# Performance work log

Measured on AMD Instinct MI355X. Metric: run time of the kernel, lower is better.

## Reference

```python
import jax, jax.numpy as jnp
import numpy as np

B, S, D, H = 1, 2048, 1024, 16
HD = D // H  # head_dim = 64
ROPE_BASE = 10000.0


def _rope_cos_sin(seqlen, head_dim, dtype):
    inv_freq = 1.0 / (ROPE_BASE ** (jnp.arange(0, head_dim, 2, dtype=jnp.float32) / head_dim))
    t = jnp.arange(seqlen, dtype=jnp.float32)
    freqs = jnp.outer(t, inv_freq)                      # [S, HD/2]
    emb = jnp.concatenate([freqs, freqs], axis=-1)      # [S, HD]
    # broadcast shape [1, S, 1, HD] over (batch, seq, heads, head_dim)
    return jnp.cos(emb)[None, :, None, :].astype(dtype), jnp.sin(emb)[None, :, None, :].astype(dtype)


def _rotate_half(x):
    x1, x2 = jnp.split(x, 2, axis=-1)
    return jnp.concatenate([-x2, x1], axis=-1)


def setup_inputs() -> dict:
    key = jax.random.key(0)
    k1, k2, k3 = jax.random.split(key, 3)
    std_in = 1.0 / np.sqrt(D)
    std_out = std_in / np.sqrt(2.0)  # layer_id = 0
    x = jax.random.normal(k1, (B, S, D), dtype=jnp.float32)
    w_in = jax.random.normal(k2, (3 * H * HD, D), dtype=jnp.float32) * std_in
    w_out = jax.random.normal(k3, (D, H * HD), dtype=jnp.float32) * std_out
    return {"x": x, "w_in": w_in, "w_out": w_out, "is_causal": 1}


def reference(x, w_in, w_out, is_causal):
    b, s, _ = x.shape
    qkv = jnp.einsum('bsd,ed->bse', x, w_in)            # [B,S,3*H*HD]
    xq, xk, xv = jnp.split(qkv, 3, axis=-1)
    xq = xq.reshape(b, s, H, HD)
    xk = xk.reshape(b, s, H, HD)
    xv = xv.reshape(b, s, H, HD)
    cos, sin = _rope_cos_sin(s, HD, xq.dtype)
    xq = xq * cos + _rotate_half(xq) * sin
    xk = xk * cos + _rotate_half(xk) * sin
    scale = 1.0 / np.sqrt(HD)
    scores = jnp.einsum('bqhd,bkhd->bhqk', xq, xk) * scale  # [B,H,S,S]
    if is_causal:
        mask = jnp.tril(jnp.ones((s, s), dtype=bool))
        scores = jnp.where(mask[None, None], scores, jnp.finfo(scores.dtype).min)
    probs = jax.nn.softmax(scores, axis=-1)
    out = jnp.einsum('bhqk,bkhd->bqhd', probs, xv)      # [B,S,H,HD]
    out = out.reshape(b, s, H * HD)
    return jnp.einsum('bse,de->bsd', out, w_out)
```

## Files before the change

kernel.cpp:

```cpp
#include <hip/hip_runtime.h>
#include <stdint.h>

#define S_LEN 2048
#define DMODEL 1024
#define NHEAD 16
#define HDIM 64
#define NE 3072
#define C2 0.18033688011112042f
#define RINV (-13.287712379549449f / 32.f)

typedef __attribute__((ext_vector_type(8))) short short8_t;
typedef __attribute__((ext_vector_type(4))) float f32x4;
typedef __attribute__((ext_vector_type(16))) float f32x16;

__device__ __forceinline__ float bf2f(ushort u) {
  union { float f; uint32_t i; } c; c.i = ((uint32_t)u) << 16; return c.f;
}
__device__ __forceinline__ ushort f2bf(float f) {
  union { float f; uint32_t i; } c; c.f = f;
  uint32_t x = c.i;
  return (ushort)((x + 0x7fffu + ((x >> 16) & 1u)) >> 16);
}

__device__ __forceinline__ void gload_lds16(const ushort* g, ushort* l) {
  __builtin_amdgcn_global_load_lds(
      (const __attribute__((address_space(1))) void*)g,
      (__attribute__((address_space(3))) void*)l, 16, 0, 0);
}

__global__ void cvt_all(const float* __restrict__ x, const float* __restrict__ w_in,
                        const float* __restrict__ w_out,
                        ushort* __restrict__ xbf, ushort* __restrict__ winbf,
                        ushort* __restrict__ woutbf) {
  int i = blockIdx.x * blockDim.x + threadIdx.x;
  const float* src; ushort* dst; int off;
  if (i < 524288)       { src = x;     dst = xbf;    off = i; }
  else if (i < 1310720) { src = w_in;  dst = winbf;  off = i - 524288; }
  else                  { src = w_out; dst = woutbf; off = i - 1310720; }
  float4 v = ((const float4*)src)[off];
  ushort4 o;
  o.x = f2bf(v.x); o.y = f2bf(v.y); o.z = f2bf(v.z); o.w = f2bf(v.w);
  ((ushort4*)dst)[off] = o;
}

template<int BM, int BN, int MODE>
__global__ __launch_bounds__(256) void gemm_abt(
    const ushort* __restrict__ A, const ushort* __restrict__ B,
    void* __restrict__ Cv, ushort* __restrict__ kfrag, ushort* __restrict__ vfrag,
    int M, int N, int K)
{
  constexpr int AR = BM / 32;
  constexpr int AC = BN / 32;
  constexpr int PG = (BM + BN) / 32;
  __shared__ ushort lds[(BM + BN) * 64];

  const int nbn = N / BN;
  const int cpx = gridDim.x >> 3;
  const int bid = blockIdx.x;
  const int swz = (bid & 7) * cpx + (bid >> 3);
  const int bm = swz / nbn;
  const int bn = swz - bm * nbn;
  const int tid = threadIdx.x;
  const int w = tid >> 6, l = tid & 63;
  const int wm = w >> 1, wn = w & 1;
  const int fr = l & 15, fg = l >> 4;

  f32x4 acc[AR][AC];
#pragma unroll
  for (int r = 0; r < AR; ++r)
#pragma unroll
    for (int c = 0; c < AC; ++c) acc[r][c] = (f32x4){0.f, 0.f, 0.f, 0.f};

  const ushort* gsrc[PG];
  ushort* ldst[PG];
#pragma unroll
  for (int i = 0; i < PG; ++i) {
    int ch = w + 4 * i;
    int row = ch * 8 + (l >> 3);
    if (row < BM)
      gsrc[i] = A + (size_t)(bm * BM + row) * K + (l & 7) * 8;
    else
      gsrc[i] = B + (size_t)(bn * BN + (row - BM)) * K + (l & 7) * 8;
    ldst[i] = &lds[ch * 512];
  }

  const ushort* fa = &lds[(wm * (BM / 2) + fr) * 64 + fg * 8];
  const ushort* fb = &lds[BM * 64 + (wn * (BN / 2) + fr) * 64 + fg * 8];

  for (int k0 = 0; k0 < K; k0 += 64) {
    __syncthreads();
#pragma unroll
    for (int i = 0; i < PG; ++i) gload_lds16(gsrc[i] + k0, ldst[i]);
    __syncthreads();

    short8_t af[AR][2], bfr[AC][2];
#pragma unroll
    for (int r = 0; r < AR; ++r)
#pragma unroll
      for (int kk = 0; kk < 2; ++kk) {
        union { short8_t v; uint4 q; } u;
        u.q = *(const uint4*)(fa + r * 1024 + kk * 32);
        af[r][kk] = u.v;
      }
#pragma unroll
    for (int c = 0; c < AC; ++c)
#pragma unroll
      for (int kk = 0; kk < 2; ++kk) {
        union { short8_t v; uint4 q; } u;
        u.q = *(const uint4*)(fb + c * 1024 + kk * 32);
        bfr[c][kk] = u.v;
      }
    __builtin_amdgcn_s_setprio(1);
#pragma unroll
    for (int kk = 0; kk < 2; ++kk)
#pragma unroll
      for (int r = 0; r < AR; ++r)
#pragma unroll
        for (int c = 0; c < AC; ++c)
          acc[r][c] = __builtin_amdgcn_mfma_f32_16x16x32_bf16(af[r][kk], bfr[c][kk], acc[r][c], 0, 0, 0);
    __builtin_amdgcn_s_setprio(0);
  }

  if constexpr (MODE == 0) {
    const int row0 = bm * BM + wm * (BM / 2) + fg * 4;
    const int col0 = bn * BN + wn * (BN / 2) + fr;
#pragma unroll
    for (int r = 0; r < AR; ++r)
#pragma unroll
      for (int c = 0; c < AC; ++c)
#pragma unroll
        for (int j = 0; j < 4; ++j)
          ((float*)Cv)[(size_t)(row0 + r * 16 + j) * N + col0 + c * 16] = acc[r][c][j];
  } else {
    const int cls = bn >> 4;
    const int h = bn & 15;
    if (cls == 0) {
      const int row0 = bm * BM + wm * (BM / 2) + fg * 4;
      const int colq = bn * 64 + wn * 32 + fr;
      ushort* qb = (ushort*)Cv;
#pragma unroll
      for (int r = 0; r < AR; ++r)
#pragma unroll
        for (int c = 0; c < AC; ++c)
#pragma unroll
          for (int j = 0; j < 4; ++j)
            qb[(size_t)(row0 + r * 16 + j) * 1024 + colq + c * 16] = f2bf(acc[r][c][j]);
    } else {
      __syncthreads();
      ushort* T = lds;
#pragma unroll
      for (int r = 0; r < AR; ++r)
#pragma unroll
        for (int c = 0; c < AC; ++c)
#pragma unroll
          for (int j = 0; j < 4; ++j) {
            int rl = wm * 64 + r * 16 + fg * 4 + j;
            int cl = wn * 32 + c * 16 + fr;
            T[rl * 72 + cl] = f2bf(acc[r][c][j]);
          }
      __syncthreads();

      if (cls == 1) {
        const int ii = tid & 31;
        const float invf = exp2f((float)ii * RINV);
#pragma unroll
        for (int kk = 0; kk < 16; ++kk) {
          int key = (tid >> 5) * 16 + kk;
          float sn, cs;
          sincosf((float)(bm * 128 + key) * invf, &sn, &cs);
          float x1 = bf2f(T[key * 72 + ii]), x2 = bf2f(T[key * 72 + ii + 32]);
          T[key * 72 + ii]      = f2bf(x1 * cs - x2 * sn);
          T[key * 72 + ii + 32] = f2bf(x2 * cs + x1 * sn);
        }
        __syncthreads();
#pragma unroll
        for (int it = 0; it < 4; ++it) {
          int idx = tid + 256 * it;
          int tt = idx >> 9, e = idx & 511;
          int c2 = e >> 6, l2 = e & 63, q2 = l2 & 31, hi2 = l2 >> 5;
          int kh = c2 >> 2, ks = c2 & 3;
          uint4 v = *(const uint4*)&T[(64 * tt + 32 * kh + q2) * 72 + 16 * ks + 8 * hi2];
          *(uint4*)(kfrag + (size_t)(h * 32 + bm * 2 + tt) * 4096 + e * 8) = v;
        }
      } else {
#pragma unroll
        for (int it = 0; it < 4; ++it) {
          int idx = tid + 256 * it;
          int tt = idx >> 9, e = idx & 511;
          int c2 = e >> 6, l2 = e & 63, q2 = l2 & 31, hi2 = l2 >> 5;
          int ks = c2 >> 1, dh = c2 & 1;
          ushort tmp[8];
#pragma unroll
          for (int jj = 0; jj < 8; ++jj)
            tmp[jj] = T[(64 * tt + 16 * ks + 8 * hi2 + jj) * 72 + 32 * dh + q2];
          *(uint4*)(vfrag + (size_t)(h * 32 + bm * 2 + tt) * 4096 + e * 8) = *(const uint4*)tmp;
        }
      }
    }
  }
}

__global__ __launch_bounds__(256) void attn_mfma(
    const ushort* __restrict__ qbuf, const ushort* __restrict__ kfrag,
    const ushort* __restrict__ vfrag, ushort* __restrict__ O,
    const int* __restrict__ icausal)
{
  __shared__ ushort obf[4][32][68];
  __shared__ float2 mdl[4][32];

  const int bid = blockIdx.x;
  const int h = (bid & 7) * 2 + ((bid >> 3) & 1);
  const int i = bid >> 4;
  const int g = i & 15, k = i >> 4;
  const int qt = (k == 0) ? g : (k == 1) ? (63 - g) : (k == 2) ? (31 - g) : (32 + g);

  const int causal = *icausal;
  const int nt = causal ? ((qt >> 1) + 1) : (S_LEN / 64);

  const int tid = threadIdx.x;
  const int w = tid >> 6, l = tid & 63;
  const int q = l & 31, hi = l >> 5;
  const int q0 = qt * 32;
  const int qa = q0 + q;
  const int t0 = w * nt / 4, t1 = (w + 1) * nt / 4;

  short8_t qf[4];
  {
    const ushort* qp = qbuf + (size_t)qa * 1024 + h * HDIM + 8 * hi;
#pragma unroll
    for (int ks = 0; ks < 4; ++ks) {
      union { short8_t v; uint4 u; } uu;
      uu.u = *(const uint4*)(qp + 16 * ks);
      qf[ks] = uu.v;
    }
    union { short8_t v; ushort u[8]; } a0, a1, b0, b1;
    a0.v = qf[0]; a1.v = qf[1]; b0.v = qf[2]; b1.v = qf[3];
#pragma unroll
    for (int j = 0; j < 8; ++j) {
      {
        float invf = exp2f((float)(8 * hi + j) * RINV);
        float sn, cs; sincosf((float)qa * invf, &sn, &cs);
        float x1 = bf2f(a0.u[j]), x2 = bf2f(b0.u[j]);
        a0.u[j] = f2bf(x1 * cs - x2 * sn);
        b0.u[j] = f2bf(x2 * cs + x1 * sn);
      }
      {
        float invf = exp2f((float)(16 + 8 * hi + j) * RINV);
        float sn, cs; sincosf((float)qa * invf, &sn, &cs);
        float x1 = bf2f(a1.u[j]), x2 = bf2f(b1.u[j]);
        a1.u[j] = f2bf(x1 * cs - x2 * sn);
        b1.u[j] = f2bf(x2 * cs + x1 * sn);
      }
    }
    qf[0] = a0.v; qf[1] = a1.v; qf[2] = b0.v; qf[3] = b1.v;
  }

  const ushort* kb = kfrag + (size_t)(h * 32 + t0) * 4096 + l * 8;
  const ushort* vb = vfrag + (size_t)(h * 32 + t0) * 4096 + l * 8;

  float m_run = -1e30f, den = 0.f;
  f32x16 oacc[2];
#pragma unroll
  for (int d = 0; d < 2; ++d)
#pragma unroll
    for (int r = 0; r < 16; ++r) oacc[d][r] = 0.f;

  if (t0 < t1) {
    uint4 kq[8];
#pragma unroll
    for (int ks = 0; ks < 4; ++ks)
#pragma unroll
      for (int kh = 0; kh < 2; ++kh)
        kq[ks * 2 + kh] = *(const uint4*)(kb + (kh * 4 + ks) * 512);
    kb += 4096;

    for (int t = t0; t < t1; ++t) {
      uint4 vq[8];
#pragma unroll
      for (int c = 0; c < 8; ++c)
        vq[c] = *(const uint4*)(vb + c * 512);
      vb += 4096;

      f32x16 sacc[2];
#pragma unroll
      for (int kh = 0; kh < 2; ++kh)
#pragma unroll
        for (int r = 0; r < 16; ++r) sacc[kh][r] = 0.f;
      __builtin_amdgcn_s_setprio(1);
#pragma unroll
      for (int ks = 0; ks < 4; ++ks)
#pragma unroll
        for (int kh = 0; kh < 2; ++kh) {
          union { short8_t v; uint4 u; } ku;
          ku.u = kq[ks * 2 + kh];
          sacc[kh] = __builtin_amdgcn_mfma_f32_32x32x16_bf16(ku.v, qf[ks], sacc[kh], 0, 0, 0);
        }
      __builtin_amdgcn_s_setprio(0);

      if (t + 1 < t1) {
#pragma unroll
        for (int ks = 0; ks < 4; ++ks)
#pragma unroll
          for (int kh = 0; kh < 2; ++kh)
            kq[ks * 2 + kh] = *(const uint4*)(kb + (kh * 4 + ks) * 512);
        kb += 4096;
      }

      if (causal && t == nt - 1) {
        const int k0 = t * 64;
#pragma unroll
        for (int kh = 0; kh < 2; ++kh)
#pragma unroll
          for (int r = 0; r < 16; ++r)
            if (k0 + 32 * kh + (r & 3) + 8 * (r >> 2) + 4 * hi > qa) sacc[kh][r] = -3e38f;
      }

      float v0 = -3e38f, v1 = -3e38f, v2 = -3e38f, v3 = -3e38f;
#pragma unroll
      for (int kh = 0; kh < 2; ++kh)
#pragma unroll
        for (int r = 0; r < 16; r += 4) {
          v0 = fmaxf(v0, sacc[kh][r + 0]);
          v1 = fmaxf(v1, sacc[kh][r + 1]);
          v2 = fmaxf(v2, sacc[kh][r + 2]);
          v3 = fmaxf(v3, sacc[kh][r + 3]);
        }
      float vmax = fmaxf(fmaxf(v0, v1), fmaxf(v2, v3));
      vmax = fmaxf(vmax, __shfl_xor(vmax, 32));

      if (__any(vmax > m_run + 44.3614196f)) {
        float mn = fmaxf(m_run, vmax);
        float alpha = exp2f((m_run - mn) * C2);
        den *= alpha;
#pragma unroll
        for (int d = 0; d < 2; ++d)
#pragma unroll
          for (int r = 0; r < 16; ++r) oacc[d][r] *= alpha;
        m_run = mn;
      }
      float mc2 = m_run * C2;
      float p0 = 0.f, p1 = 0.f, p2 = 0.f, p3 = 0.f;
#pragma unroll
      for (int kh = 0; kh < 2; ++kh)
#pragma unroll
        for (int r = 0; r < 16; r += 4) {
          float e0 = exp2f(fmaf(sacc[kh][r + 0], C2, -mc2));
          float e1 = exp2f(fmaf(sacc[kh][r + 1], C2, -mc2));
          float e2 = exp2f(fmaf(sacc[kh][r + 2], C2, -mc2));
          float e3 = exp2f(fmaf(sacc[kh][r + 3], C2, -mc2));
          sacc[kh][r + 0] = e0; sacc[kh][r + 1] = e1;
          sacc[kh][r + 2] = e2; sacc[kh][r + 3] = e3;
          p0 += e0; p1 += e1; p2 += e2; p3 += e3;
        }
      float psum = (p0 + p1) + (p2 + p3);
      psum += __shfl_xor(psum, 32);
      den += psum;

      short8_t pa[4];
#pragma unroll
      for (int ks = 0; ks < 4; ++ks) {
        const int blk = ks >> 1, kp = (ks & 1) * 8;
        uint wL0, wL1, wH0, wH1;
        asm("v_cvt_pk_bf16_f32 %0, %1, %2" : "=v"(wL0) : "v"(sacc[blk][kp + 0]), "v"(sacc[blk][kp + 1]));
        asm("v_cvt_pk_bf16_f32 %0, %1, %2" : "=v"(wL1) : "v"(sacc[blk][kp + 2]), "v"(sacc[blk][kp + 3]));
        asm("v_cvt_pk_bf16_f32 %0, %1, %2" : "=v"(wH0) : "v"(sacc[blk][kp + 4]), "v"(sacc[blk][kp + 5]));
        asm("v_cvt_pk_bf16_f32 %0, %1, %2" : "=v"(wH1) : "v"(sacc[blk][kp + 6]), "v"(sacc[blk][kp + 7]));
        uint s0 = hi ? wL0 : wH0, s1 = hi ? wL1 : wH1;
        uint r0 = __shfl_xor(s0, 32), r1 = __shfl_xor(s1, 32);
        union { short8_t v; uint u[4]; } pu;
        pu.u[0] = hi ? r0 : wL0;
        pu.u[1] = hi ? r1 : wL1;
        pu.u[2] = hi ? wH0 : r0;
        pu.u[3] = hi ? wH1 : r1;
        pa[ks] = pu.v;
      }

      __builtin_amdgcn_s_setprio(1);
#pragma unroll
      for (int ks = 0; ks < 4; ++ks)
#pragma unroll
        for (int dh = 0; dh < 2; ++dh) {
          union { short8_t v; uint4 u; } vu;
          vu.u = vq[ks * 2 + dh];
          oacc[dh] = __builtin_amdgcn_mfma_f32_32x32x16_bf16(vu.v, pa[ks], oacc[dh], 0, 0, 0);
        }
      __builtin_amdgcn_s_setprio(0);
    }
  }

#pragma unroll
  for (int dh = 0; dh < 2; ++dh)
#pragma unroll
    for (int rq = 0; rq < 4; ++rq) {
      uint a0, a1;
      asm("v_cvt_pk_bf16_f32 %0, %1, %2" : "=v"(a0) : "v"(oacc[dh][4 * rq + 0]), "v"(oacc[dh][4 * rq + 1]));
      asm("v_cvt_pk_bf16_f32 %0, %1, %2" : "=v"(a1) : "v"(oacc[dh][4 * rq + 2]), "v"(oacc[dh][4 * rq + 3]));
      uint2 dd; dd.x = a0; dd.y = a1;
      *(uint2*)&obf[w][q][32 * dh + 8 * rq + 4 * hi] = dd;
    }
  if (hi == 0) mdl[w][q] = make_float2(m_run, den);
  __syncthreads();

  {
    const int qq = tid >> 3, d8 = tid & 7;
    float2 md0 = mdl[0][qq], md1 = mdl[1][qq], md2 = mdl[2][qq], md3 = mdl[3][qq];
    float mt = fmaxf(fmaxf(md0.x, md1.x), fmaxf(md2.x, md3.x));
    float w0 = exp2f((md0.x - mt) * C2);
    float w1 = exp2f((md1.x - mt) * C2);
    float w2 = exp2f((md2.x - mt) * C2);
    float w3 = exp2f((md3.x - mt) * C2);
    float inv = 1.f / (md0.y * w0 + md1.y * w1 + md2.y * w2 + md3.y * w3);

    uint4 a = *(const uint4*)&obf[0][qq][d8 * 8];
    uint4 b = *(const uint4*)&obf[1][qq][d8 * 8];
    uint4 c = *(const uint4*)&obf[2][qq][d8 * 8];
    uint4 d = *(const uint4*)&obf[3][qq][d8 * 8];
    const ushort* ap = (const ushort*)&a;
    const ushort* bp = (const ushort*)&b;
    const ushort* cp = (const ushort*)&c;
    const ushort* dp = (const ushort*)&d;
    ushort out8[8];
#pragma unroll
    for (int e = 0; e < 8; ++e) {
      float acc = bf2f(ap[e]) * w0 + bf2f(bp[e]) * w1 + bf2f(cp[e]) * w2 + bf2f(dp[e]) * w3;
      out8[e] = f2bf(acc * inv);
    }
    *(uint4*)(O + (size_t)(q0 + qq) * DMODEL + h * HDIM + d8 * 8) = *(const uint4*)out8;
  }
}

extern "C" void kernel_launch(void* const* d_in, const int* in_sizes, int n_in,
                              void* d_out, int out_size, void* d_ws, size_t ws_size,
                              hipStream_t stream) {
  const float* x     = (const float*)d_in[0];
  const float* w_in  = (const float*)d_in[1];
  const float* w_out = (const float*)d_in[2];
  const int* icausal = (const int*)d_in[3];

  char* ws = (char*)d_ws;
  ushort* xbf    = (ushort*)(ws);
  ushort* winbf  = (ushort*)(ws + 4194304);
  ushort* woutbf = (ushort*)(ws + 10485760);
  ushort* qbuf   = (ushort*)(ws + 12582912);
  ushort* kfrag  = (ushort*)(ws + 16777216);
  ushort* vfrag  = (ushort*)(ws + 20971520);
  ushort* obuf   = (ushort*)(ws + 25165824);

  cvt_all<<<6144, 256, 0, stream>>>(x, w_in, w_out, xbf, winbf, woutbf);

  gemm_abt<128, 64, 2><<<16 * 48, 256, 0, stream>>>(xbf, winbf, (void*)qbuf, kfrag, vfrag, 2048, 3072, 1024);
  attn_mfma<<<1024, 256, 0, stream>>>(qbuf, kfrag, vfrag, obuf, icausal);
  gemm_abt<64, 64, 0><<<32 * 16, 256, 0, stream>>>(obuf, woutbf, d_out, nullptr, nullptr, 2048, 1024, 1024);
}
```

Before: 81.49 us.

## Software-pipeline QK^T MFMA for next tile with softmax and PV of current

Restructures the attention inner loop so the QK^T MFMAs for tile t+1 are issued after the softmax of tile t and before its PV MFMAs. The K fragments for tile t+2 and the V fragments for tile t+1 are prefetched further ahead. The exp2 computation is folded into the bf16 packing loop to shorten live ranges. Launch bounds now request two blocks per CU. The aim is to overlap matrix-core work with the exp/shuffle softmax ALU work and to hide global load latency, at the cost of more live registers (sacc, kq and vq all held across the iteration).

```diff
diff --git a/kernel.cpp b/kernel.cpp
--- a/kernel.cpp
+++ b/kernel.cpp
@@ -200,7 +200,7 @@
   }
 }
 
-__global__ __launch_bounds__(256) void attn_mfma(
+__global__ __launch_bounds__(256, 2) void attn_mfma(
     const ushort* __restrict__ qbuf, const ushort* __restrict__ kfrag,
     const ushort* __restrict__ vfrag, ushort* __restrict__ O,
     const int* __restrict__ icausal)
@@ -266,45 +266,45 @@
     for (int r = 0; r < 16; ++r) oacc[d][r] = 0.f;
 
   if (t0 < t1) {
-    uint4 kq[8];
+    uint4 kq[8], vq[8];
 #pragma unroll
     for (int ks = 0; ks < 4; ++ks)
 #pragma unroll
       for (int kh = 0; kh < 2; ++kh)
         kq[ks * 2 + kh] = *(const uint4*)(kb + (kh * 4 + ks) * 512);
     kb += 4096;
+#pragma unroll
+    for (int c = 0; c < 8; ++c)
+      vq[c] = *(const uint4*)(vb + c * 512);
+    vb += 4096;
+
+    f32x16 sacc[2];
+#pragma unroll
+    for (int kh = 0; kh < 2; ++kh)
+#pragma unroll
+      for (int r = 0; r < 16; ++r) sacc[kh][r] = 0.f;
+    __builtin_amdgcn_s_setprio(1);
+#pragma unroll
+    for (int ks = 0; ks < 4; ++ks)
+#pragma unroll
+      for (int kh = 0; kh < 2; ++kh) {
+        union { short8_t v; uint4 u; } ku;
+        ku.u = kq[ks * 2 + kh];
+        sacc[kh] = __builtin_amdgcn_mfma_f32_32x32x16_bf16(ku.v, qf[ks], sacc[kh], 0, 0, 0);
+      }
+    __builtin_amdgcn_s_setprio(0);
+
+    if (t0 + 1 < t1) {
+#pragma unroll
+      for (int ks = 0; ks < 4; ++ks)
+#pragma unroll
+        for (int kh = 0; kh < 2; ++kh)
+          kq[ks * 2 + kh] = *(const uint4*)(kb + (kh * 4 + ks) * 512);
+      kb += 4096;
+    }
 
     for (int t = t0; t < t1; ++t) {
-      uint4 vq[8];
-#pragma unroll
-      for (int c = 0; c < 8; ++c)
-        vq[c] = *(const uint4*)(vb + c * 512);
-      vb += 4096;
-
-      f32x16 sacc[2];
-#pragma unroll
-      for (int kh = 0; kh < 2; ++kh)
-#pragma unroll
-        for (int r = 0; r < 16; ++r) sacc[kh][r] = 0.f;
-      __builtin_amdgcn_s_setprio(1);
-#pragma unroll
-      for (int ks = 0; ks < 4; ++ks)
-#pragma unroll
-        for (int kh = 0; kh < 2; ++kh) {
-          union { short8_t v; uint4 u; } ku;
-          ku.u = kq[ks * 2 + kh];
-          sacc[kh] = __builtin_amdgcn_mfma_f32_32x32x16_bf16(ku.v, qf[ks], sacc[kh], 0, 0, 0);
-        }
-      __builtin_amdgcn_s_setprio(0);
-
-      if (t + 1 < t1) {
-#pragma unroll
-        for (int ks = 0; ks < 4; ++ks)
-#pragma unroll
-          for (int kh = 0; kh < 2; ++kh)
-            kq[ks * 2 + kh] = *(const uint4*)(kb + (kh * 4 + ks) * 512);
-        kb += 4096;
-      }
+      const bool more = (t + 1 < t1);
 
       if (causal && t == nt - 1) {
         const int k0 = t * 64;
@@ -338,33 +338,27 @@
           for (int r = 0; r < 16; ++r) oacc[d][r] *= alpha;
         m_run = mn;
       }
+
       float mc2 = m_run * C2;
       float p0 = 0.f, p1 = 0.f, p2 = 0.f, p3 = 0.f;
-#pragma unroll
-      for (int kh = 0; kh < 2; ++kh)
-#pragma unroll
-        for (int r = 0; r < 16; r += 4) {
-          float e0 = exp2f(fmaf(sacc[kh][r + 0], C2, -mc2));
-          float e1 = exp2f(fmaf(sacc[kh][r + 1], C2, -mc2));
-          float e2 = exp2f(fmaf(sacc[kh][r + 2], C2, -mc2));
-          float e3 = exp2f(fmaf(sacc[kh][r + 3], C2, -mc2));
-          sacc[kh][r + 0] = e0; sacc[kh][r + 1] = e1;
-          sacc[kh][r + 2] = e2; sacc[kh][r + 3] = e3;
-          p0 += e0; p1 += e1; p2 += e2; p3 += e3;
-        }
-      float psum = (p0 + p1) + (p2 + p3);
-      psum += __shfl_xor(psum, 32);
-      den += psum;
-
       short8_t pa[4];
 #pragma unroll
       for (int ks = 0; ks < 4; ++ks) {
         const int blk = ks >> 1, kp = (ks & 1) * 8;
+        float e0 = exp2f(fmaf(sacc[blk][kp + 0], C2, -mc2));
+        float e1 = exp2f(fmaf(sacc[blk][kp + 1], C2, -mc2));
+        float e2 = exp2f(fmaf(sacc[blk][kp + 2], C2, -mc2));
+        float e3 = exp2f(fmaf(sacc[blk][kp + 3], C2, -mc2));
+        float e4 = exp2f(fmaf(sacc[blk][kp + 4], C2, -mc2));
+        float e5 = exp2f(fmaf(sacc[blk][kp + 5], C2, -mc2));
+        float e6 = exp2f(fmaf(sacc[blk][kp + 6], C2, -mc2));
+        float e7 = exp2f(fmaf(sacc[blk][kp + 7], C2, -mc2));
+        p0 += e0 + e4; p1 += e1 + e5; p2 += e2 + e6; p3 += e3 + e7;
         uint wL0, wL1, wH0, wH1;
-        asm("v_cvt_pk_bf16_f32 %0, %1, %2" : "=v"(wL0) : "v"(sacc[blk][kp + 0]), "v"(sacc[blk][kp + 1]));
-        asm("v_cvt_pk_bf16_f32 %0, %1, %2" : "=v"(wL1) : "v"(sacc[blk][kp + 2]), "v"(sacc[blk][kp + 3]));
-        asm("v_cvt_pk_bf16_f32 %0, %1, %2" : "=v"(wH0) : "v"(sacc[blk][kp + 4]), "v"(sacc[blk][kp + 5]));
-        asm("v_cvt_pk_bf16_f32 %0, %1, %2" : "=v"(wH1) : "v"(sacc[blk][kp + 6]), "v"(sacc[blk][kp + 7]));
+        asm("v_cvt_pk_bf16_f32 %0, %1, %2" : "=v"(wL0) : "v"(e0), "v"(e1));
+        asm("v_cvt_pk_bf16_f32 %0, %1, %2" : "=v"(wL1) : "v"(e2), "v"(e3));
+        asm("v_cvt_pk_bf16_f32 %0, %1, %2" : "=v"(wH0) : "v"(e4), "v"(e5));
+        asm("v_cvt_pk_bf16_f32 %0, %1, %2" : "=v"(wH1) : "v"(e6), "v"(e7));
         uint s0 = hi ? wL0 : wH0, s1 = hi ? wL1 : wH1;
         uint r0 = __shfl_xor(s0, 32), r1 = __shfl_xor(s1, 32);
         union { short8_t v; uint u[4]; } pu;
@@ -374,6 +368,35 @@
         pu.u[3] = hi ? wH1 : r1;
         pa[ks] = pu.v;
       }
+      float psum = (p0 + p1) + (p2 + p3);
+      psum += __shfl_xor(psum, 32);
+      den += psum;
+
+      if (more) {
+#pragma unroll
+        for (int kh = 0; kh < 2; ++kh)
+#pragma unroll
+          for (int r = 0; r < 16; ++r) sacc[kh][r] = 0.f;
+        __builtin_amdgcn_s_setprio(1);
+#pragma unroll
+        for (int ks = 0; ks < 4; ++ks)
+#pragma unroll
+          for (int kh = 0; kh < 2; ++kh) {
+            union { short8_t v; uint4 u; } ku;
+            ku.u = kq[ks * 2 + kh];
+            sacc[kh] = __builtin_amdgcn_mfma_f32_32x32x16_bf16(ku.v, qf[ks], sacc[kh], 0, 0, 0);
+          }
+        __builtin_amdgcn_s_setprio(0);
+      }
+
+      if (t + 2 < t1) {
+#pragma unroll
+        for (int ks = 0; ks < 4; ++ks)
+#pragma unroll
+          for (int kh = 0; kh < 2; ++kh)
+            kq[ks * 2 + kh] = *(const uint4*)(kb + (kh * 4 + ks) * 512);
+        kb += 4096;
+      }
 
       __builtin_amdgcn_s_setprio(1);
 #pragma unroll
@@ -385,6 +408,13 @@
           oacc[dh] = __builtin_amdgcn_mfma_f32_32x32x16_bf16(vu.v, pa[ks], oacc[dh], 0, 0, 0);
         }
       __builtin_amdgcn_s_setprio(0);
+
+      if (more) {
+#pragma unroll
+        for (int c = 0; c < 8; ++c)
+          vq[c] = *(const uint4*)(vb + c * 512);
+        vb += 4096;
+      }
     }
   }
 
```

Result: slower. 83.43 us (+2.4%).
